# Kernel optimization log

Hardware: AMD Instinct MI355X
Metric: run time of the kernel (lower is better)

The kernel has to match this reference:

```python
import jax, jax.numpy as jnp
import numpy as np
from jax import lax


def _avg_pool(x, k, p):
    # torch avg_pool2d with count_include_pad=True: sum over window / k*k
    s = lax.reduce_window(x, 0.0, lax.add, (1, 1, k, k), (1, 1, 1, 1),
                          ((0, 0), (0, 0), (p, p), (p, p)))
    return s / float(k * k)


def setup_inputs() -> dict:
    key = jax.random.key(0)
    k1, k2, k3, k4 = jax.random.split(key, 4)
    B, H, W = 4, 512, 512
    hcc = 16
    C = 2 * hcc  # color channels = 2*half_color_channels
    mask = jax.random.normal(k1, (B, 16, H, W), jnp.float32)
    color = jax.random.normal(k2, (B, C, H, W), jnp.float32)
    w_bbx = jax.random.normal(k3, (C, 1, 5, 5), jnp.float32) * 0.1   # depthwise 5x5, groups=C
    w_score = jax.random.normal(k4, (1, C, 1, 1), jnp.float32) * 0.1  # 1x1 conv -> 1 channel
    return {"mask": mask, "color": color, "w_bbx": w_bbx, "w_score": w_score}


def reference(mask, color, w_bbx, w_score):
    B, C, H, W = color.shape
    col = _avg_pool(color, 3, 1)
    wh = lax.conv_general_dilated(col, w_bbx, (1, 1), ((2, 2), (2, 2)),
                                  dimension_numbers=('NCHW', 'OIHW', 'NCHW'),
                                  feature_group_count=C)  # [B,C,H,W]
    wmax = wh[:, 0::2].max(axis=1, keepdims=True)
    hmax = wh[:, 1::2].max(axis=1, keepdims=True)
    sc = lax.conv_general_dilated(color, w_score, (1, 1), 'VALID',
                                  dimension_numbers=('NCHW', 'OIHW', 'NCHW'))
    sc = _avg_pool(sc, 5, 2)
    sc = _avg_pool(sc, 3, 1)
    bbx = jnp.concatenate([sc, wmax, hmax], axis=1)  # [B,3,H,W]

    # --- FeatureHead decode ---
    score_map = bbx[:, 0:1]                      # [B,1,H,W]
    flat = bbx.transpose(0, 2, 3, 1).reshape(B, H * W, 3)
    s = jax.nn.sigmoid(flat[:, :, 0])            # [B,HW]
    w = flat[:, :, 0]   # bug-faithful: original uses channel 0 (score) for w
    h = flat[:, :, 1]   # and channel 1 for h
    _, top_idx = lax.top_k(s, 10)                # [B,10]
    m = jnp.zeros((B, H * W), bool).at[jnp.arange(B)[:, None], top_idx].set(True)
    m = (m & (s > 0.6)) | (s > 0.9)
    ys = jnp.repeat(jnp.arange(H, dtype=jnp.float32), W)  # [HW]
    xs = jnp.tile(jnp.arange(W, dtype=jnp.float32), H)    # [HW]
    wv = jnp.exp(w) * 10.0
    hv = jnp.exp(h) * 10.0
    x1 = jnp.floor(xs - wv)
    x2 = jnp.ceil(xs + wv)
    y1 = jnp.floor(ys - hv)
    y2 = jnp.ceil(ys + hv)
    # static-shape equivalent of boolean compaction: dense [B,HW,5], rows
    # zeroed where not selected (mask m marks the selected boxes).
    out = jnp.stack([s, x1, y1, x2, y2], axis=-1)
    out = jnp.where(m[..., None], out, 0.0)
    return (score_map, out, m)
```

## Files before the change

kernel.cpp:

```cpp
#include <hip/hip_runtime.h>
#include <math.h>

#define H 512
#define W 512
#define HW (H*W)
#define NB 4
#define NC 32

__device__ __forceinline__ void gload_lds16(const void* g, void* l) {
    __builtin_amdgcn_global_load_lds((const __attribute__((address_space(1))) void*)g,
                                     (__attribute__((address_space(3))) void*)l, 16, 0, 0);
}

__global__ __launch_bounds__(256) void k_whmax_sc(const float* __restrict__ color,
                                                  const float* __restrict__ wbbx,
                                                  const float* __restrict__ wscore,
                                                  const float* __restrict__ zp,
                                                  float* __restrict__ pw,
                                                  float* __restrict__ scE) {
    __shared__ float A[38][140];
    __shared__ float P[36][136];

    const int t  = threadIdx.x;
    const int X0 = blockIdx.x * 128;
    const int Y0 = blockIdx.y * 32;
    const int b  = blockIdx.z >> 2;
    const int g  = blockIdx.z & 3;
    const int tx = t & 31, ty = t >> 5;

    size_t goff[6];
    bool   inb[6], act[6];
    #pragma unroll
    for (int k = 0; k < 6; ++k) {
        int u = t + k * 256;
        act[k] = (u < 38 * 35);
        int r = u / 35, c4 = u % 35;
        int gy = Y0 - 3 + r, gx0 = X0 - 4 + c4 * 4;
        inb[k]  = act[k] && (gy >= 0) && (gy < H) && (gx0 >= 0) && (gx0 <= W - 4);
        goff[k] = (size_t)(gy < 0 ? 0 : gy) * W + (gx0 < 0 ? 0 : gx0);
    }
    char* Abase = (char*)&A[0][0];

    float wmx[4][4], scacc[4][4];
    #pragma unroll
    for (int ol = 0; ol < 4; ++ol)
        #pragma unroll
        for (int cc = 0; cc < 4; ++cc) { wmx[ol][cc] = -INFINITY; scacc[ol][cc] = 0.f; }

    for (int ci = 0; ci < 4; ++ci) {
        const int ce = 8 * g + 2 * ci;
        const int co = ce + 1;
        const float* img  = color + ((size_t)b * NC + ce) * HW;
        const float* imgO = color + ((size_t)b * NC + co) * HW;
        const float* wc   = wbbx + ce * 25;
        const float wse   = wscore[ce];
        const float wso   = wscore[co];

        #pragma unroll
        for (int k = 0; k < 6; ++k) {
            if (act[k]) {
                const float* src = inb[k] ? (img + goff[k]) : zp;
                void* dst = Abase + (size_t)((t & ~63) + k * 256) * 16;
                gload_lds16(src, dst);
            }
        }

        float4 ov[4];
        #pragma unroll
        for (int ol = 0; ol < 4; ++ol)
            ov[ol] = *(const float4*)(imgO + (size_t)(Y0 + ty * 4 + ol) * W + X0 + tx * 4);
        #pragma unroll
        for (int ol = 0; ol < 4; ++ol) {
            scacc[ol][0] = fmaf(ov[ol].x, wso, scacc[ol][0]);
            scacc[ol][1] = fmaf(ov[ol].y, wso, scacc[ol][1]);
            scacc[ol][2] = fmaf(ov[ol].z, wso, scacc[ol][2]);
            scacc[ol][3] = fmaf(ov[ol].w, wso, scacc[ol][3]);
        }

        __syncthreads();

        #pragma unroll
        for (int ol = 0; ol < 4; ++ol) {
            float4 v = *(const float4*)&A[3 + ty * 4 + ol][4 + tx * 4];
            scacc[ol][0] = fmaf(v.x, wse, scacc[ol][0]);
            scacc[ol][1] = fmaf(v.y, wse, scacc[ol][1]);
            scacc[ol][2] = fmaf(v.z, wse, scacc[ol][2]);
            scacc[ol][3] = fmaf(v.w, wse, scacc[ol][3]);
        }

        for (int u = t; u < 36 * 34; u += 256) {
            int pr = u / 34, ch = u % 34;
            int j0 = ch * 4;
            int gyP = Y0 - 2 + pr;
            float4 pv = make_float4(0.f, 0.f, 0.f, 0.f);
            if (gyP >= 0 && gyP < H) {
                float vs[8];
                float4 a0 = *(const float4*)&A[pr + 0][j0 + 0];
                float4 b0 = *(const float4*)&A[pr + 0][j0 + 4];
                float4 a1 = *(const float4*)&A[pr + 1][j0 + 0];
                float4 b1 = *(const float4*)&A[pr + 1][j0 + 4];
                float4 a2 = *(const float4*)&A[pr + 2][j0 + 0];
                float4 b2 = *(const float4*)&A[pr + 2][j0 + 4];
                vs[0] = a0.x + a1.x + a2.x;
                vs[1] = a0.y + a1.y + a2.y;
                vs[2] = a0.z + a1.z + a2.z;
                vs[3] = a0.w + a1.w + a2.w;
                vs[4] = b0.x + b1.x + b2.x;
                vs[5] = b0.y + b1.y + b2.y;
                vs[6] = b0.z + b1.z + b2.z;
                vs[7] = b0.w + b1.w + b2.w;
                float p[4];
                #pragma unroll
                for (int jj = 0; jj < 4; ++jj) {
                    int gxP = X0 - 2 + j0 + jj;
                    float s = (vs[jj + 1] + vs[jj + 2] + vs[jj + 3]) * (1.f / 9.f);
                    p[jj] = (gxP >= 0 && gxP < W) ? s : 0.f;
                }
                pv = make_float4(p[0], p[1], p[2], p[3]);
            }
            *(float4*)&P[pr][j0] = pv;
        }
        __syncthreads();

        float acc[4][4];
        #pragma unroll
        for (int ol = 0; ol < 4; ++ol)
            #pragma unroll
            for (int cc = 0; cc < 4; ++cc) acc[ol][cc] = 0.f;

        #pragma unroll
        for (int pr8 = 0; pr8 < 8; ++pr8) {
            int pr = ty * 4 + pr8;
            float4 q0 = *(const float4*)&P[pr][tx * 4 + 0];
            float4 q1 = *(const float4*)&P[pr][tx * 4 + 4];
            float c8[8] = {q0.x, q0.y, q0.z, q0.w, q1.x, q1.y, q1.z, q1.w};
            #pragma unroll
            for (int ol = 0; ol < 4; ++ol) {
                const int ky = pr8 - ol;
                if (ky >= 0 && ky <= 4) {
                    #pragma unroll
                    for (int cc = 0; cc < 4; ++cc) {
                        float a = acc[ol][cc];
                        #pragma unroll
                        for (int kx = 0; kx < 5; ++kx)
                            a = fmaf(c8[cc + kx], wc[ky * 5 + kx], a);
                        acc[ol][cc] = a;
                    }
                }
            }
        }
        #pragma unroll
        for (int ol = 0; ol < 4; ++ol)
            #pragma unroll
            for (int cc = 0; cc < 4; ++cc)
                wmx[ol][cc] = fmaxf(wmx[ol][cc], acc[ol][cc]);
    }

    size_t off = ((size_t)g * NB + b) * HW + (size_t)(Y0 + ty * 4) * W + X0 + tx * 4;
    #pragma unroll
    for (int ol = 0; ol < 4; ++ol) {
        *(float4*)(pw  + off + (size_t)ol * W) = make_float4(wmx[ol][0], wmx[ol][1], wmx[ol][2], wmx[ol][3]);
        *(float4*)(scE + off + (size_t)ol * W) = make_float4(scacc[ol][0], scacc[ol][1], scacc[ol][2], scacc[ol][3]);
    }
}

__global__ __launch_bounds__(256) void k_poolcand(const float* __restrict__ scE,
                                                  float* __restrict__ score_map,
                                                  float* __restrict__ cand) {
    const int xh = blockIdx.x;
    const int sb = blockIdx.y;
    const int b  = blockIdx.z;
    const int t  = threadIdx.x;
    const int y0 = sb * 8;
    const int C0 = xh * 256;

    __shared__ float A[14][264];
    __shared__ float Bf[14][264];

    for (int r = 0; r < 14; ++r) {
        int gy = y0 - 3 + r;
        for (int l = t; l < 264; l += 256) {
            int gx = C0 - 4 + l;
            float v = 0.f;
            if (gy >= 0 && gy < H && gx >= 0 && gx < W) {
                size_t idx = (size_t)b * HW + (size_t)gy * W + gx;
                v = scE[idx] + scE[(size_t)NB * HW + idx]
                  + scE[(size_t)2 * NB * HW + idx] + scE[(size_t)3 * NB * HW + idx];
            }
            A[r][l] = v;
        }
    }
    __syncthreads();
    for (int r = 0; r < 14; ++r)
        for (int l = 2 + t; l < 262; l += 256)
            Bf[r][l] = A[r][l - 2] + A[r][l - 1] + A[r][l] + A[r][l + 1] + A[r][l + 2];
    __syncthreads();
    for (int r2 = 0; r2 < 10; ++r2) {
        int gy = y0 - 1 + r2;
        for (int l = 2 + t; l < 262; l += 256) {
            int gx = C0 - 4 + l;
            float s = 0.f;
            if (gy >= 0 && gy < H && gx >= 0 && gx < W) {
                #pragma unroll
                for (int d = 0; d < 5; ++d) s += Bf[r2 + d][l];
                s *= (1.f / 25.f);
            }
            A[r2][l] = s;
        }
    }
    __syncthreads();
    for (int r2 = 0; r2 < 10; ++r2)
        for (int l = 3 + t; l < 261; l += 256)
            Bf[r2][l] = A[r2][l - 1] + A[r2][l] + A[r2][l + 1];
    __syncthreads();

    float top[10];
    #pragma unroll
    for (int k = 0; k < 10; ++k) top[k] = -INFINITY;

    const int l = 4 + t;
    for (int r3 = 0; r3 < 8; ++r3) {
        float sv = (Bf[r3][l] + Bf[r3 + 1][l] + Bf[r3 + 2][l]) * (1.f / 9.f);
        score_map[(size_t)b * HW + (size_t)(y0 + r3) * W + C0 + t] = sv;
        float s = 1.f / (1.f + expf(-sv));
        if (s > top[9]) {
            top[9] = s;
            #pragma unroll
            for (int k = 9; k > 0; --k)
                if (top[k] > top[k - 1]) { float tmp = top[k - 1]; top[k - 1] = top[k]; top[k] = tmp; }
        }
    }

    __shared__ float sv_[256];
    __shared__ int   si_[256];
    __shared__ int   swin;
    int ptr = 0;
    for (int r = 0; r < 10; ++r) {
        sv_[t] = (ptr < 10) ? top[ptr] : -INFINITY;
        si_[t] = t;
        __syncthreads();
        for (int off = 128; off > 0; off >>= 1) {
            if (t < off && sv_[t + off] > sv_[t]) { sv_[t] = sv_[t + off]; si_[t] = si_[t + off]; }
            __syncthreads();
        }
        if (t == 0) { cand[(((size_t)b * 64 + sb) * 2 + xh) * 10 + r] = sv_[0]; swin = si_[0]; }
        __syncthreads();
        if (t == swin) ptr++;
        __syncthreads();
    }
}

__global__ __launch_bounds__(256) void k_v10(const float* __restrict__ cand, float* __restrict__ v10) {
    const int b = blockIdx.x, t = threadIdx.x;
    __shared__ float c[1280];
    __shared__ float wv[4];
    __shared__ int   wi[4];
    for (int j = t; j < 1280; j += 256) c[j] = cand[b * 1280 + j];
    __syncthreads();
    for (int r = 0; r < 10; ++r) {
        float bv = -INFINITY; int bi = 0;
        #pragma unroll
        for (int k = 0; k < 5; ++k) {
            int j = t + k * 256;
            float v = c[j];
            if (v > bv) { bv = v; bi = j; }
        }
        #pragma unroll
        for (int off = 32; off > 0; off >>= 1) {
            float ovv = __shfl_down(bv, off);
            int   ovi = __shfl_down(bi, off);
            if (ovv > bv) { bv = ovv; bi = ovi; }
        }
        if ((t & 63) == 0) { wv[t >> 6] = bv; wi[t >> 6] = bi; }
        __syncthreads();
        if (t == 0) {
            float m = wv[0]; int mi = wi[0];
            #pragma unroll
            for (int w = 1; w < 4; ++w) if (wv[w] > m) { m = wv[w]; mi = wi[w]; }
            c[mi] = -INFINITY;
            if (r == 9) v10[b] = m;
        }
        __syncthreads();
    }
}

__global__ __launch_bounds__(256) void k_final(const float* __restrict__ smap,
                                               const float* __restrict__ pw,
                                               const float* __restrict__ v10,
                                               float* __restrict__ outbuf,
                                               float* __restrict__ mbuf) {
    __shared__ float st[1280];
    const int t = threadIdx.x;
    const int p = blockIdx.x * 256 + t;
    int b = p / HW, i = p % HW;
    float scv = smap[p];
    float s   = 1.f / (1.f + expf(-scv));
    float s10 = v10[b];
    bool  m   = (s >= s10 && s > 0.6f) || (s > 0.9f);
    size_t idx = (size_t)b * HW + i;
    float wmv = fmaxf(fmaxf(pw[idx], pw[(size_t)NB * HW + idx]),
                      fmaxf(pw[(size_t)2 * NB * HW + idx], pw[(size_t)3 * NB * HW + idx]));
    float wv = expf(scv) * 10.f;
    float hv = expf(wmv) * 10.f;
    float xs = (float)(i & (W - 1));
    float ys = (float)(i >> 9);
    float o0 = 0.f, o1 = 0.f, o2 = 0.f, o3 = 0.f, o4 = 0.f;
    if (m) {
        o0 = s;
        o1 = floorf(xs - wv);
        o2 = floorf(ys - hv);
        o3 = ceilf(xs + wv);
        o4 = ceilf(ys + hv);
    }
    st[t * 5 + 0] = o0; st[t * 5 + 1] = o1; st[t * 5 + 2] = o2;
    st[t * 5 + 3] = o3; st[t * 5 + 4] = o4;
    mbuf[p] = m ? 1.f : 0.f;
    __syncthreads();
    float4* ob4 = (float4*)(outbuf + (size_t)blockIdx.x * 1280);
    const float4* s4 = (const float4*)st;
    ob4[t] = s4[t];
    if (t < 64) ob4[256 + t] = s4[256 + t];
}

extern "C" void kernel_launch(void* const* d_in, const int* in_sizes, int n_in,
                              void* d_out, int out_size, void* d_ws, size_t ws_size,
                              hipStream_t stream) {
    const float* color  = (const float*)d_in[1];
    const float* wbbx   = (const float*)d_in[2];
    const float* wscore = (const float*)d_in[3];

    float* out       = (float*)d_out;
    float* score_map = out;
    float* outbuf    = out + 1048576;
    float* mbuf      = out + 1048576 + 5242880;

    float* ws   = (float*)d_ws;
    float* pw   = ws;
    float* scE  = ws + (size_t)4 * NB * HW;
    float* cand = ws + (size_t)8 * NB * HW;
    float* v10  = cand + 5120;
    float* zp   = cand + 8192;

    hipMemsetAsync(zp, 0, 256, stream);

    k_whmax_sc <<<dim3(4, 16, NB * 4), 256, 0, stream>>>(color, wbbx, wscore, zp, pw, scE);
    k_poolcand <<<dim3(2, 64, NB), 256, 0, stream>>>(scE, score_map, cand);
    k_v10      <<<4, 256, 0, stream>>>(cand, v10);
    k_final    <<<(NB * HW) / 256, 256, 0, stream>>>(score_map, pw, v10, outbuf, mbuf);
}
```

Measured before the change: 93.17 us.

## Double-buffer color tile loads and fuse avg-pool into per-thread conv

```diff
diff --git a/kernel.cpp b/kernel.cpp
--- a/kernel.cpp
+++ b/kernel.cpp
@@ -18,8 +18,7 @@
                                                   const float* __restrict__ zp,
                                                   float* __restrict__ pw,
                                                   float* __restrict__ scE) {
-    __shared__ float A[38][140];
-    __shared__ float P[36][136];
+    __shared__ float A[2][38][140];
 
     const int t  = threadIdx.x;
     const int X0 = blockIdx.x * 128;
@@ -39,36 +38,58 @@
         inb[k]  = act[k] && (gy >= 0) && (gy < H) && (gx0 >= 0) && (gx0 <= W - 4);
         goff[k] = (size_t)(gy < 0 ? 0 : gy) * W + (gx0 < 0 ? 0 : gx0);
     }
-    char* Abase = (char*)&A[0][0];
+
+    auto stage = [&](int c, int buf) {
+        const float* img = color + ((size_t)b * NC + c) * HW;
+        char* Abase = (char*)&A[buf][0][0];
+        #pragma unroll
+        for (int k = 0; k < 6; ++k) {
+            if (act[k]) {
+                const float* src = inb[k] ? (img + goff[k]) : zp;
+                gload_lds16(src, Abase + (size_t)((t & ~63) + k * 256) * 16);
+            }
+        }
+    };
+
+    float cmask[8];
+    #pragma unroll
+    for (int j = 0; j < 8; ++j) {
+        int gx = X0 + tx * 4 - 2 + j;
+        cmask[j] = (gx >= 0 && gx < W) ? (1.f / 9.f) : 0.f;
+    }
+    bool rmask[8];
+    #pragma unroll
+    for (int q = 0; q < 8; ++q) {
+        int gy = Y0 + ty * 4 - 2 + q;
+        rmask[q] = (gy >= 0 && gy < H);
+    }
 
     float wmx[4][4], scacc[4][4];
     #pragma unroll
     for (int ol = 0; ol < 4; ++ol)
         #pragma unroll
         for (int cc = 0; cc < 4; ++cc) { wmx[ol][cc] = -INFINITY; scacc[ol][cc] = 0.f; }
+
+    stage(8 * g, 0);
+    int cur = 0;
 
     for (int ci = 0; ci < 4; ++ci) {
         const int ce = 8 * g + 2 * ci;
         const int co = ce + 1;
-        const float* img  = color + ((size_t)b * NC + ce) * HW;
-        const float* imgO = color + ((size_t)b * NC + co) * HW;
         const float* wc   = wbbx + ce * 25;
         const float wse   = wscore[ce];
         const float wso   = wscore[co];
-
-        #pragma unroll
-        for (int k = 0; k < 6; ++k) {
-            if (act[k]) {
-                const float* src = inb[k] ? (img + goff[k]) : zp;
-                void* dst = Abase + (size_t)((t & ~63) + k * 256) * 16;
-                gload_lds16(src, dst);
-            }
-        }
+        const float* imgO = color + ((size_t)b * NC + co) * HW;
 
         float4 ov[4];
         #pragma unroll
         for (int ol = 0; ol < 4; ++ol)
             ov[ol] = *(const float4*)(imgO + (size_t)(Y0 + ty * 4 + ol) * W + X0 + tx * 4);
+
+        __syncthreads();
+
+        if (ci < 3) stage(ce + 2, cur ^ 1);
+
         #pragma unroll
         for (int ol = 0; ol < 4; ++ol) {
             scacc[ol][0] = fmaf(ov[ol].x, wso, scacc[ol][0]);
@@ -77,74 +98,54 @@
             scacc[ol][3] = fmaf(ov[ol].w, wso, scacc[ol][3]);
         }
 
-        __syncthreads();
-
         #pragma unroll
         for (int ol = 0; ol < 4; ++ol) {
-            float4 v = *(const float4*)&A[3 + ty * 4 + ol][4 + tx * 4];
+            float4 v = *(const float4*)&A[cur][3 + ty * 4 + ol][4 + tx * 4];
             scacc[ol][0] = fmaf(v.x, wse, scacc[ol][0]);
             scacc[ol][1] = fmaf(v.y, wse, scacc[ol][1]);
             scacc[ol][2] = fmaf(v.z, wse, scacc[ol][2]);
             scacc[ol][3] = fmaf(v.w, wse, scacc[ol][3]);
         }
 
-        for (int u = t; u < 36 * 34; u += 256) {
-            int pr = u / 34, ch = u % 34;
-            int j0 = ch * 4;
-            int gyP = Y0 - 2 + pr;
-            float4 pv = make_float4(0.f, 0.f, 0.f, 0.f);
-            if (gyP >= 0 && gyP < H) {
-                float vs[8];
-                float4 a0 = *(const float4*)&A[pr + 0][j0 + 0];
-                float4 b0 = *(const float4*)&A[pr + 0][j0 + 4];
-                float4 a1 = *(const float4*)&A[pr + 1][j0 + 0];
-                float4 b1 = *(const float4*)&A[pr + 1][j0 + 4];
-                float4 a2 = *(const float4*)&A[pr + 2][j0 + 0];
-                float4 b2 = *(const float4*)&A[pr + 2][j0 + 4];
-                vs[0] = a0.x + a1.x + a2.x;
-                vs[1] = a0.y + a1.y + a2.y;
-                vs[2] = a0.z + a1.z + a2.z;
-                vs[3] = a0.w + a1.w + a2.w;
-                vs[4] = b0.x + b1.x + b2.x;
-                vs[5] = b0.y + b1.y + b2.y;
-                vs[6] = b0.z + b1.z + b2.z;
-                vs[7] = b0.w + b1.w + b2.w;
-                float p[4];
+        float acc[4][4];
+        #pragma unroll
+        for (int ol = 0; ol < 4; ++ol)
+            #pragma unroll
+            for (int cc = 0; cc < 4; ++cc) acc[ol][cc] = 0.f;
+
+        float rs[3][8];
+        #pragma unroll
+        for (int rr = 0; rr < 10; ++rr) {
+            float4 a4 = *(const float4*)&A[cur][ty * 4 + rr][tx * 4 + 0];
+            float4 b4 = *(const float4*)&A[cur][ty * 4 + rr][tx * 4 + 4];
+            float4 c4 = *(const float4*)&A[cur][ty * 4 + rr][tx * 4 + 8];
+            float v[12] = {a4.x, a4.y, a4.z, a4.w, b4.x, b4.y, b4.z, b4.w, c4.x, c4.y, c4.z, c4.w};
+            float* rsc = rs[rr % 3];
+            #pragma unroll
+            for (int j = 0; j < 8; ++j) rsc[j] = v[j + 1] + v[j + 2] + v[j + 3];
+            if (rr >= 2) {
+                const int q = rr - 2;
+                float pooled[8];
+                if (rmask[q]) {
+                    #pragma unroll
+                    for (int j = 0; j < 8; ++j)
+                        pooled[j] = (rs[(rr - 2) % 3][j] + rs[(rr - 1) % 3][j] + rs[rr % 3][j]) * cmask[j];
+                } else {
+                    #pragma unroll
+                    for (int j = 0; j < 8; ++j) pooled[j] = 0.f;
+                }
                 #pragma unroll
-                for (int jj = 0; jj < 4; ++jj) {
-                    int gxP = X0 - 2 + j0 + jj;
-                    float s = (vs[jj + 1] + vs[jj + 2] + vs[jj + 3]) * (1.f / 9.f);
-                    p[jj] = (gxP >= 0 && gxP < W) ? s : 0.f;
-                }
-                pv = make_float4(p[0], p[1], p[2], p[3]);
-            }
-            *(float4*)&P[pr][j0] = pv;
-        }
-        __syncthreads();
-
-        float acc[4][4];
-        #pragma unroll
-        for (int ol = 0; ol < 4; ++ol)
-            #pragma unroll
-            for (int cc = 0; cc < 4; ++cc) acc[ol][cc] = 0.f;
-
-        #pragma unroll
-        for (int pr8 = 0; pr8 < 8; ++pr8) {
-            int pr = ty * 4 + pr8;
-            float4 q0 = *(const float4*)&P[pr][tx * 4 + 0];
-            float4 q1 = *(const float4*)&P[pr][tx * 4 + 4];
-            float c8[8] = {q0.x, q0.y, q0.z, q0.w, q1.x, q1.y, q1.z, q1.w};
-            #pragma unroll
-            for (int ol = 0; ol < 4; ++ol) {
-                const int ky = pr8 - ol;
-                if (ky >= 0 && ky <= 4) {
-                    #pragma unroll
-                    for (int cc = 0; cc < 4; ++cc) {
-                        float a = acc[ol][cc];
+                for (int ol = 0; ol < 4; ++ol) {
+                    const int ky = q - ol;
+                    if (ky >= 0 && ky <= 4) {
                         #pragma unroll
-                        for (int kx = 0; kx < 5; ++kx)
-                            a = fmaf(c8[cc + kx], wc[ky * 5 + kx], a);
-                        acc[ol][cc] = a;
+                        for (int cc = 0; cc < 4; ++cc) {
+                            float a = acc[ol][cc];
+                            #pragma unroll
+                            for (int kx = 0; kx < 5; ++kx)
+                                a = fmaf(pooled[cc + kx], wc[ky * 5 + kx], a);
+                            acc[ol][cc] = a;
+                        }
                     }
                 }
             }
@@ -154,6 +155,8 @@
             #pragma unroll
             for (int cc = 0; cc < 4; ++cc)
                 wmx[ol][cc] = fmaxf(wmx[ol][cc], acc[ol][cc]);
+
+        cur ^= 1;
     }
 
     size_t off = ((size_t)g * NB + b) * HW + (size_t)(Y0 + ty * 4) * W + X0 + tx * 4;
```

Measured after the change: 98.61 us. +5.8%, slower.
